# Kernel tuning notes

Measured on AMD Instinct MI355X. Metric: run time of the kernel, lower is better.

The kernel has to match this reference:

```python
import jax, jax.numpy as jnp
import numpy as np

N = 262144       # number of samples
DIM = 64         # feature dim
NCLASSES = 128   # number of gaussian classes


def setup_inputs() -> dict:
    key = jax.random.key(0)
    k1, k2, k3, k4 = jax.random.split(key, 4)
    inputs = jax.random.normal(k1, (N, DIM), dtype=jnp.float32)
    target = jax.random.randint(k2, (N,), 0, NCLASSES)
    mean_param = jax.random.normal(k3, (NCLASSES, DIM), dtype=jnp.float32) * 0.02
    cov_param = jax.random.normal(k4, (NCLASSES, DIM, DIM), dtype=jnp.float32) * 0.02
    return {"inputs": inputs, "target": target,
            "mean_param": mean_param, "cov_param": cov_param}


def _l2_distance(sample_mean, sample_cov_sq, mean_param, cov_param):
    # Concrete stand-in for the user-supplied `distance` callable:
    # squared-L2 between the empirical class mean and the learned means,
    # plus the energy of the empirical covariance vector and learned covariances.
    return (jnp.sum((sample_mean[None, :] - mean_param) ** 2)
            + sample_cov_sq
            + jnp.sum(cov_param ** 2))


def reference(inputs, target, mean_param, cov_param):
    nclasses = mean_param.shape[0]
    n = inputs.shape[0]
    # per-class counts and means (fused segmented reduction, one pass)
    counts = jax.ops.segment_sum(jnp.ones((n,), inputs.dtype), target,
                                 num_segments=nclasses)           # [C]
    sums = jax.ops.segment_sum(inputs, target, num_segments=nclasses)  # [C, D]
    means = sums / counts[:, None]                                 # [C, D]
    # center each sample by its class mean  (torch: temp = x - mean)
    temp = inputs - means[target]                                  # [N, D]
    # torch: cov = mm(temp, temp.T).mean(0); row k equals temp_k . mean_j(temp_j)
    # so we only need the per-class sum of centered rows (analytically ~0).
    s = jax.ops.segment_sum(temp, target, num_segments=nclasses)   # [C, D]
    cov = jnp.sum(temp * s[target], axis=-1) / counts[target]      # [N] per-sample entry
    # loss in the python loop is overwritten each iter -> only last class survives
    last = nclasses - 1
    cov_sq_last = jax.ops.segment_sum(cov * cov, target, num_segments=nclasses)[last]
    loss = _l2_distance(means[last], cov_sq_last, mean_param, cov_param)
    return loss
```

## Files before the change

kernel.cpp:

```cpp
#include <hip/hip_runtime.h>


#define DIM 64
#define NCLASSES 128
#define LAST (NCLASSES - 1)
#define NBLOCKS 64
#define SLOT 72
#define FLAG_MAGIC 0x5CA1AB1Eu

__global__ __launch_bounds__(256) void gem_onenode(
    const float* __restrict__ inputs, const int* __restrict__ target,
    const float* __restrict__ mean_param, const float* __restrict__ cov_param,
    int n, int cov_n4, float* __restrict__ ws, float* __restrict__ out)
{
    const int tid  = threadIdx.x;
    const int lane = tid & 63;
    const int wib  = tid >> 6;
    const int b    = blockIdx.x;
    const int gwave = b * 4 + wib;
    const int nwaves = NBLOCKS * 4;

    float acc = 0.f;
    int   cnt = 0;
    for (int cb = gwave * 64; cb < n; cb += nwaves * 64) {
        int t = target[cb + lane];
        unsigned long long m = __ballot(t == LAST);
        cnt += __popcll(m);
        while (m) {
            int i = __ffsll(m) - 1;
            m &= m - 1;
            acc += inputs[(size_t)(cb + i) * DIM + lane];
        }
    }

    const float4* c4 = (const float4*)cov_param;
    float csum = 0.f;
    for (int i = b * 256 + tid; i < cov_n4; i += NBLOCKS * 256) {
        float4 v = c4[i];
        csum += v.x * v.x + v.y * v.y + v.z * v.z + v.w * v.w;
    }
    for (int off = 32; off; off >>= 1) csum += __shfl_down(csum, off, 64);

    __shared__ float sacc[4][DIM];
    __shared__ float scov[4];
    __shared__ int   scnt[4];
    sacc[wib][lane] = acc;
    if (lane == 0) { scov[wib] = csum; scnt[wib] = cnt; }
    __syncthreads();

    float* slot = ws + (size_t)b * SLOT;
    if (wib == 0) slot[lane] = sacc[0][lane] + sacc[1][lane] + sacc[2][lane] + sacc[3][lane];
    if (tid == 0) {
        slot[DIM]     = (float)(scnt[0] + scnt[1] + scnt[2] + scnt[3]);
        slot[DIM + 1] = scov[0] + scov[1] + scov[2] + scov[3];
    }
    __threadfence();
    __syncthreads();
    if (tid == 0)
        __hip_atomic_store((unsigned int*)(slot + DIM + 2), FLAG_MAGIC,
                           __ATOMIC_RELEASE, __HIP_MEMORY_SCOPE_AGENT);

    if (b != NBLOCKS - 1) return;

    if (tid < NBLOCKS) {
        unsigned int* f = (unsigned int*)(ws + (size_t)tid * SLOT + DIM + 2);
        while (__hip_atomic_load(f, __ATOMIC_ACQUIRE, __HIP_MEMORY_SCOPE_AGENT)
               != FLAG_MAGIC) {}
    }
    __syncthreads();

    __shared__ float rr[4][DIM];
    __shared__ float smean[DIM];
    __shared__ float scount, scovsq;
    float s = 0.f;
    for (int bb = wib; bb < NBLOCKS; bb += 4)
        s += __hip_atomic_load(ws + (size_t)bb * SLOT + lane,
                               __ATOMIC_RELAXED, __HIP_MEMORY_SCOPE_AGENT);
    rr[wib][lane] = s;
    if (wib == 1) {
        float c = __hip_atomic_load(ws + (size_t)lane * SLOT + DIM,
                                    __ATOMIC_RELAXED, __HIP_MEMORY_SCOPE_AGENT);
        for (int off = 32; off; off >>= 1) c += __shfl_down(c, off, 64);
        if (lane == 0) scount = c;
    }
    if (wib == 2) {
        float c = __hip_atomic_load(ws + (size_t)lane * SLOT + DIM + 1,
                                    __ATOMIC_RELAXED, __HIP_MEMORY_SCOPE_AGENT);
        for (int off = 32; off; off >>= 1) c += __shfl_down(c, off, 64);
        if (lane == 0) scovsq = c;
    }
    __syncthreads();
    if (wib == 0) smean[lane] = (rr[0][lane] + rr[1][lane] + rr[2][lane] + rr[3][lane]) / scount;
    __syncthreads();

    float dacc = 0.f;
    for (int i = tid; i < NCLASSES * DIM; i += 256) {
        float d = smean[i & (DIM - 1)] - mean_param[i];
        dacc += d * d;
    }
    for (int off = 32; off; off >>= 1) dacc += __shfl_down(dacc, off, 64);
    __shared__ float fr[4];
    if (lane == 0) fr[wib] = dacc;
    __syncthreads();
    if (tid == 0) out[0] = fr[0] + fr[1] + fr[2] + fr[3] + scovsq;
}

extern "C" void kernel_launch(void* const* d_in, const int* in_sizes, int n_in,
                              void* d_out, int out_size, void* d_ws, size_t ws_size,
                              hipStream_t stream) {
    const float* inputs     = (const float*)d_in[0];
    const int*   target     = (const int*)d_in[1];
    const float* mean_param = (const float*)d_in[2];
    const float* cov_param  = (const float*)d_in[3];
    float* out = (float*)d_out;
    float* ws  = (float*)d_ws;

    const int n     = in_sizes[0] / DIM;
    const int cov_n = in_sizes[3];

    gem_onenode<<<NBLOCKS, 256, 0, stream>>>(inputs, target, mean_param, cov_param,
                                             n, cov_n / 4, ws, out);
}
```

Measured before the change: 116.5 us.

## Quadruple grid size and vectorize target scan with int4 loads and four ballots

Raises the block count from 64 to 256 so the target scan, row gathers and cov_param sum-of-squares spread over more CUs. Each wave now reads 256 targets per step through int4 loads and runs four ballots, and gathers matching rows at offset 4*bit+j. The last block now waits on flags from all 256 blocks, with every thread spinning, and sums 256 count and covariance partials. The trade-off is a longer serial gather and spin-wait in the final block against more memory-level parallelism in the scan.

```diff
diff --git a/kernel.cpp b/kernel.cpp
--- a/kernel.cpp
+++ b/kernel.cpp
@@ -4,7 +4,7 @@
 #define DIM 64
 #define NCLASSES 128
 #define LAST (NCLASSES - 1)
-#define NBLOCKS 64
+#define NBLOCKS 256
 #define SLOT 72
 #define FLAG_MAGIC 0x5CA1AB1Eu
 
@@ -17,19 +17,26 @@
     const int lane = tid & 63;
     const int wib  = tid >> 6;
     const int b    = blockIdx.x;
-    const int gwave = b * 4 + wib;
+    const int gwave  = b * 4 + wib;
     const int nwaves = NBLOCKS * 4;
 
     float acc = 0.f;
     int   cnt = 0;
-    for (int cb = gwave * 64; cb < n; cb += nwaves * 64) {
-        int t = target[cb + lane];
-        unsigned long long m = __ballot(t == LAST);
-        cnt += __popcll(m);
-        while (m) {
-            int i = __ffsll(m) - 1;
-            m &= m - 1;
-            acc += inputs[(size_t)(cb + i) * DIM + lane];
+    for (int base = gwave * 256; base < n; base += nwaves * 256) {
+        const int4 t4 = *(const int4*)(target + base + lane * 4);
+        unsigned long long m0 = __ballot(t4.x == LAST);
+        unsigned long long m1 = __ballot(t4.y == LAST);
+        unsigned long long m2 = __ballot(t4.z == LAST);
+        unsigned long long m3 = __ballot(t4.w == LAST);
+        cnt += __popcll(m0) + __popcll(m1) + __popcll(m2) + __popcll(m3);
+        #pragma unroll
+        for (int j = 0; j < 4; ++j) {
+            unsigned long long m = (j == 0) ? m0 : (j == 1) ? m1 : (j == 2) ? m2 : m3;
+            while (m) {
+                int bit = __ffsll(m) - 1;
+                m &= m - 1;
+                acc += inputs[(size_t)(base + 4 * bit + j) * DIM + lane];
+            }
         }
     }
 
@@ -62,7 +69,7 @@
 
     if (b != NBLOCKS - 1) return;
 
-    if (tid < NBLOCKS) {
+    {
         unsigned int* f = (unsigned int*)(ws + (size_t)tid * SLOT + DIM + 2);
         while (__hip_atomic_load(f, __ATOMIC_ACQUIRE, __HIP_MEMORY_SCOPE_AGENT)
                != FLAG_MAGIC) {}
@@ -78,14 +85,20 @@
                                __ATOMIC_RELAXED, __HIP_MEMORY_SCOPE_AGENT);
     rr[wib][lane] = s;
     if (wib == 1) {
-        float c = __hip_atomic_load(ws + (size_t)lane * SLOT + DIM,
-                                    __ATOMIC_RELAXED, __HIP_MEMORY_SCOPE_AGENT);
+        float c = 0.f;
+        #pragma unroll
+        for (int k = 0; k < 4; ++k)
+            c += __hip_atomic_load(ws + (size_t)(lane + 64 * k) * SLOT + DIM,
+                                   __ATOMIC_RELAXED, __HIP_MEMORY_SCOPE_AGENT);
         for (int off = 32; off; off >>= 1) c += __shfl_down(c, off, 64);
         if (lane == 0) scount = c;
     }
     if (wib == 2) {
-        float c = __hip_atomic_load(ws + (size_t)lane * SLOT + DIM + 1,
-                                    __ATOMIC_RELAXED, __HIP_MEMORY_SCOPE_AGENT);
+        float c = 0.f;
+        #pragma unroll
+        for (int k = 0; k < 4; ++k)
+            c += __hip_atomic_load(ws + (size_t)(lane + 64 * k) * SLOT + DIM + 1,
+                                   __ATOMIC_RELAXED, __HIP_MEMORY_SCOPE_AGENT);
         for (int off = 32; off; off >>= 1) c += __shfl_down(c, off, 64);
         if (lane == 0) scovsq = c;
     }
```

Result: slower. 134.7 us (+15.6%).
